# Performance work log

Measured on AMD Instinct MI355X. Metric: run time of the kernel, lower is better.

Reference implementation:

```python
import jax, jax.numpy as jnp
import numpy as np

B, SEQ, DIM = 2, 4096, 1024
E, S = 8, 512          # num_slots = seq_len // num_experts
HID = 4 * DIM          # FeedForward hidden: dim * mult
SCALE = DIM ** 0.5     # RMSNorm scale


def rmsnorm(x, gamma):
    # matches F.normalize(x, dim=-1) * dim**0.5 * gamma (eps=1e-12 clamp on the norm)
    n = jnp.linalg.norm(x, axis=-1, keepdims=True)
    return x / jnp.maximum(n, 1e-12) * SCALE * gamma


def setup_inputs() -> dict:
    key = jax.random.key(0)
    ks = jax.random.split(key, 4)
    w_init = lambda k, shape: jax.random.normal(k, shape, dtype=jnp.float32) * 0.02
    return {
        "x": jax.random.normal(ks[0], (B, SEQ, DIM), dtype=jnp.float32),
        "norm_gamma": jnp.ones((DIM,), jnp.float32),
        "slot_norm_gamma": jnp.ones((DIM,), jnp.float32),
        "slot_embeds": jax.random.normal(ks[1], (E, S, DIM), dtype=jnp.float32),
        "w1": w_init(ks[2], (E, DIM, HID)),
        "b1": jnp.zeros((E, HID), jnp.float32),
        "w2": w_init(ks[3], (E, HID, DIM)),
        "b2": jnp.zeros((E, DIM), jnp.float32),
    }


def reference(x, norm_gamma, slot_norm_gamma, slot_embeds, w1, b1, w2, b2):
    xn = rmsnorm(x, norm_gamma)                 # [b, n, d]
    sn = rmsnorm(slot_embeds, slot_norm_gamma)  # [e, s, d]

    logits = jnp.einsum('bnd,esd->bnes', xn, sn)                   # [b, n, e, s]
    dispatch = jax.nn.softmax(logits, axis=1)                      # softmax over tokens n
    b, n, e, s = logits.shape
    combine = jax.nn.softmax(logits.reshape(b, n, e * s), axis=-1) # softmax over (e s)

    slots = jnp.einsum('bnd,bnes->besd', xn, dispatch)             # [b, e, s, d]

    # per-expert FeedForward: Linear -> GELU(exact) -> Linear (dropout=0)
    h = jnp.einsum('besd,edh->besh', slots, w1) + b1[None, :, None, :]
    h = jax.nn.gelu(h, approximate=False)
    eo = jnp.einsum('besh,ehd->besd', h, w2) + b2[None, :, None, :]

    eo = eo.reshape(b, e * s, DIM)                                 # [b, (e s), d]
    out = jnp.einsum('bmd,bnm->bnd', eo, combine)                  # [b, n, d]
    return out
```

## Files before the change

### kernel.cpp

```cpp
#include <hip/hip_runtime.h>
#include <math.h>

#define SEQ    4096
#define DIM    1024
#define NEXP   8
#define NSLOT  512
#define ES     4096
#define HID    4096
#define NB     2
#define RMS_SCALE 32.0f

typedef __attribute__((ext_vector_type(4))) float f32x4;
typedef __attribute__((ext_vector_type(8))) short bf16x8;
typedef __attribute__((ext_vector_type(4))) unsigned short us4;

__device__ __forceinline__ unsigned short f2bf(float f) {
    unsigned u = __float_as_uint(f);
    u += 0x7fff + ((u >> 16) & 1);
    return (unsigned short)(u >> 16);
}
__device__ __forceinline__ float bf2f(unsigned short h) {
    return __uint_as_float(((unsigned)h) << 16);
}
__device__ __forceinline__ float gelu_exact(float x) {
    return 0.5f * x * (1.0f + erff(x * 0.70710678118654752f));
}

#define GLOAD_LDS16(gp, lp) \
    __builtin_amdgcn_global_load_lds((const __attribute__((address_space(1))) void*)(gp), \
                                     (__attribute__((address_space(3))) void*)(lp), 16, 0, 0)

__device__ __forceinline__ unsigned ldsoff(const void* p) {
    return (unsigned)(size_t)(const __attribute__((address_space(3))) void*)p;
}

#define DSR(dst, base, off) asm volatile("ds_read_b128 %0, %1 offset:" off : "=v"(dst) : "v"(base))
#define VM(n) asm volatile("s_waitcnt vmcnt(" #n ")" ::: "memory")
#define BAR __builtin_amdgcn_s_barrier()
#define SCB __builtin_amdgcn_sched_barrier(0)

#define PH_OPEN  SCB; BAR; asm volatile("s_waitcnt lgkmcnt(0)" ::: "memory"); SCB; \
                 __builtin_amdgcn_s_setprio(1);
#define PH_CLOSE __builtin_amdgcn_s_setprio(0); SCB;

template<int ORDER>
__global__ void rmsnorm_split(const float* __restrict__ in, const float* __restrict__ gamma,
                              unsigned short* __restrict__ outc) {
    int row = blockIdx.x;
    int t = threadIdx.x;
    float4 v = reinterpret_cast<const float4*>(in + (size_t)row * DIM)[t];
    float ss = v.x*v.x + v.y*v.y + v.z*v.z + v.w*v.w;
    #pragma unroll
    for (int off = 32; off >= 1; off >>= 1) ss += __shfl_down(ss, off, 64);
    __shared__ float red[4];
    if ((t & 63) == 0) red[t >> 6] = ss;
    __syncthreads();
    float inv = RMS_SCALE / fmaxf(sqrtf(red[0] + red[1] + red[2] + red[3]), 1e-12f);
    float4 g = reinterpret_cast<const float4*>(gamma)[t];
    float f[4] = {v.x*inv*g.x, v.y*inv*g.y, v.z*inv*g.z, v.w*inv*g.w};
    us4 hv, lv;
    #pragma unroll
    for (int q = 0; q < 4; ++q) {
        unsigned short h = f2bf(f[q]);
        hv[q] = h;
        lv[q] = f2bf(f[q] - bf2f(h));
    }
    unsigned short* rb = outc + (size_t)row * 3072;
    *reinterpret_cast<us4*>(&rb[t*4]) = hv;
    if (ORDER == 0) {
        *reinterpret_cast<us4*>(&rb[1024 + t*4]) = hv;
        *reinterpret_cast<us4*>(&rb[2048 + t*4]) = lv;
    } else {
        *reinterpret_cast<us4*>(&rb[1024 + t*4]) = lv;
        *reinterpret_cast<us4*>(&rb[2048 + t*4]) = hv;
    }
}

__global__ void col_stats_partial(const float* __restrict__ logits,
                                  float* __restrict__ pmax, float* __restrict__ psum) {
    int col = blockIdx.x * 256 + threadIdx.x;
    int ch  = blockIdx.y;
    int b   = blockIdx.z;
    const float* base = logits + ((size_t)b * SEQ + (size_t)ch * 512) * ES + col;
    float m = -INFINITY, s = 0.f;
    for (int n = 0; n < 512; ++n) {
        float v = base[(size_t)n * ES];
        float mn = fmaxf(m, v);
        s = s * __expf(m - mn) + __expf(v - mn);
        m = mn;
    }
    size_t idx = ((size_t)b * 8 + ch) * ES + col;
    pmax[idx] = m; psum[idx] = s;
}

__global__ void col_stats_reduce(const float* __restrict__ pmax, const float* __restrict__ psum,
                                 float* __restrict__ cmax, float* __restrict__ cinv) {
    int col = blockIdx.x * 256 + threadIdx.x;
    int b   = blockIdx.y;
    float m = -INFINITY, s = 0.f;
    for (int ch = 0; ch < 8; ++ch) {
        size_t idx = ((size_t)b * 8 + ch) * ES + col;
        float m2 = pmax[idx], s2 = psum[idx];
        float mn = fmaxf(m, m2);
        s = s * __expf(m - mn) + s2 * __expf(m2 - mn);
        m = mn;
    }
    cmax[(size_t)b * ES + col] = m;
    cinv[(size_t)b * ES + col] = 1.0f / s;
}

__global__ void row_stats(const float* __restrict__ logits,
                          float* __restrict__ rmax, float* __restrict__ rinv) {
    int row = blockIdx.x;
    int t = threadIdx.x;
    const float* base = logits + (size_t)row * ES;
    float m = -INFINITY, s = 0.f;
    for (int i = t; i < ES; i += 256) {
        float v = base[i];
        float mn = fmaxf(m, v);
        s = s * __expf(m - mn) + __expf(v - mn);
        m = mn;
    }
    __shared__ float sm[256], ssum[256];
    sm[t] = m; ssum[t] = s;
    __syncthreads();
    for (int off = 128; off >= 1; off >>= 1) {
        if (t < off) {
            float m1 = sm[t], m2 = sm[t+off], s1 = ssum[t], s2 = ssum[t+off];
            float mn = fmaxf(m1, m2);
            sm[t] = mn;
            ssum[t] = s1 * __expf(m1 - mn) + s2 * __expf(m2 - mn);
        }
        __syncthreads();
    }
    if (t == 0) { rmax[row] = sm[0]; rinv[row] = 1.0f / ssum[0]; }
}

__global__ void make_weights(const float* __restrict__ logits,
                             const float* __restrict__ cmax, const float* __restrict__ cinv,
                             const float* __restrict__ rmax, const float* __restrict__ rinv,
                             unsigned short* __restrict__ comb, unsigned short* __restrict__ dispT) {
    int b = blockIdx.z;
    const float* L = logits + (size_t)b * SEQ * ES;
    int n0 = blockIdx.y * 32, e0 = blockIdx.x * 32;
    int t = threadIdx.x;
    int r = t >> 3, c4 = (t & 7) * 4;
    __shared__ unsigned short tile[32][36];
    float4 v = *reinterpret_cast<const float4*>(&L[(size_t)(n0 + r) * ES + e0 + c4]);
    float rm = rmax[b*SEQ + n0 + r], ri = rinv[b*SEQ + n0 + r];
    float vv[4] = {v.x, v.y, v.z, v.w};
    us4 cb;
    #pragma unroll
    for (int q = 0; q < 4; ++q) {
        cb[q] = f2bf(__expf(vv[q] - rm) * ri);
        float dv = __expf(vv[q] - cmax[b*ES + e0 + c4 + q]) * cinv[b*ES + e0 + c4 + q];
        tile[c4 + q][r] = f2bf(dv);
    }
    *reinterpret_cast<us4*>(&comb[(size_t)b*SEQ*ES + (size_t)(n0 + r)*ES + e0 + c4]) = cb;
    __syncthreads();
    us4 o = *reinterpret_cast<us4*>(&tile[t >> 3][(t & 7) * 4]);
    *reinterpret_cast<us4*>(&dispT[(size_t)b*ES*SEQ + (size_t)(e0 + (t >> 3))*SEQ + n0 + (t & 7)*4]) = o;
}

__global__ void transpose_b16(const unsigned short* __restrict__ src, unsigned short* __restrict__ dst,
                              int sld, int dld, long sStride, long dStride) {
    int z = blockIdx.z;
    const unsigned short* S = src + (size_t)z * sStride;
    unsigned short* D = dst + (size_t)z * dStride;
    int r0 = blockIdx.y * 32, c0 = blockIdx.x * 32;
    int t = threadIdx.x;
    __shared__ unsigned short tile[32][36];
    us4 v = *reinterpret_cast<const us4*>(&S[(size_t)(r0 + (t>>3)) * sld + c0 + (t&7)*4]);
    #pragma unroll
    for (int q = 0; q < 4; ++q) tile[(t&7)*4 + q][t>>3] = v[q];
    __syncthreads();
    us4 o = *reinterpret_cast<us4*>(&tile[t >> 3][(t & 7) * 4]);
    *reinterpret_cast<us4*>(&D[(size_t)(c0 + (t>>3)) * dld + r0 + (t&7)*4]) = o;
}

__global__ void transpose_f32_b16(const float* __restrict__ src, unsigned short* __restrict__ dst,
                                  int sld, int dld, long sStride, long dStride) {
    int z = blockIdx.z;
    const float* S = src + (size_t)z * sStride;
    unsigned short* D = dst + (size_t)z * dStride;
    int r0 = blockIdx.y * 32, c0 = blockIdx.x * 32;
    int t = threadIdx.x;
    __shared__ unsigned short tile[32][36];
    float4 v = *reinterpret_cast<const float4*>(&S[(size_t)(r0 + (t>>3)) * sld + c0 + (t&7)*4]);
    float vv[4] = {v.x, v.y, v.z, v.w};
    #pragma unroll
    for (int q = 0; q < 4; ++q) tile[(t&7)*4 + q][t>>3] = f2bf(vv[q]);
    __syncthreads();
    us4 o = *reinterpret_cast<us4*>(&tile[t >> 3][(t & 7) * 4]);
    *reinterpret_cast<us4*>(&D[(size_t)(c0 + (t>>3)) * dld + r0 + (t&7)*4]) = o;
}

template<int EPI, int OM>
__global__ __launch_bounds__(512, 2)
void mfma_gemm256(const unsigned short* __restrict__ A, const unsigned short* __restrict__ B,
                  void* __restrict__ Cv, const float* __restrict__ bias,
                  int N, int K, int lda, int ldb, int ldc,
                  long aStride, long bStride, long cStride, int bMod) {
    __shared__ unsigned short lds[65536];
    const int t = threadIdx.x;
    const int lane = t & 63, wave = t >> 6;
    const int wr = wave >> 2, wc = wave & 3;
    const int z = blockIdx.z, zb = z % bMod;
    const unsigned short* Ab = A + (size_t)z * aStride;
    const unsigned short* Bb = B + (size_t)zb * bStride;
    const int gx = gridDim.x;
    int flat = blockIdx.x + blockIdx.y * gx;
    const int cpx = (gx * gridDim.y) >> 3;
    flat = (flat & 7) * cpx + (flat >> 3);
    const int m0 = (flat / gx) * 256, n0 = (flat % gx) * 256;

    const int sr = t >> 3;
    const int sg = (t & 7) ^ (sr & 7);
    const unsigned short* gA = Ab + (size_t)(m0 + sr) * lda + sg * 8;
    const int srB = sr + (sr & 32);
    const unsigned short* gB = Bb + (size_t)(n0 + srB) * ldb + sg * 8;
    unsigned short* ldsw = lds + wave * 512;

    const int lr = lane & 15, lk = lane >> 4;
    const unsigned sw0 = (unsigned)(((lk)     ^ (lr & 7)) << 4);
    const unsigned sw1 = (unsigned)(((4 + lk) ^ (lr & 7)) << 4);
    const unsigned l0  = ldsoff(lds);
    const unsigned arow = (unsigned)((wr*64 + lr) * 128);
    const unsigned brow = (unsigned)((wc*32 + lr) * 128);
    const unsigned ab00 = l0 + arow + sw0,          ab10 = l0 + arow + sw1;
    const unsigned bb00 = l0 + 32768 + brow + sw0,  bb10 = l0 + 32768 + brow + sw1;
    const unsigned ab01 = ab00 + 65536, ab11 = ab10 + 65536;
    const unsigned bb01 = bb00 + 65536, bb11 = bb10 + 65536;

    #define STAGE_A(buf, half, tt) do { \
        const unsigned short* _g = gA + (size_t)((half)*64) * lda + (tt)*64; \
        unsigned short* _l = ldsw + (buf)*32768 + (half)*8192; \
        GLOAD_LDS16(_g, _l); \
        GLOAD_LDS16(_g + (size_t)128*lda, _l + 4096); } while(0)
    #define STAGE_B(buf, half, tt) do { \
        const unsigned short* _g = gB + (size_t)((half)*32) * ldb + (tt)*64; \
        unsigned short* _l = ldsw + (buf)*32768 + 16384 + (half)*8192; \
        GLOAD_LDS16(_g, _l); \
        GLOAD_LDS16(_g + (size_t)128*ldb, _l + 4096); } while(0)

    #define MFMA16(MB, CN) \
        _Pragma("unroll") \
        for (int m = 0; m < 4; ++m) { \
            _Pragma("unroll") \
            for (int n = 0; n < 2; ++n) { \
                acc[(MB)+m][(CN)+n] = __builtin_amdgcn_mfma_f32_16x16x32_bf16(a0[m], b0[(CN)+n], acc[(MB)+m][(CN)+n], 0, 0, 0); \
                acc[(MB)+m][(CN)+n] = __builtin_amdgcn_mfma_f32_16x16x32_bf16(a1[m], b1[(CN)+n], acc[(MB)+m][(CN)+n], 0, 0, 0); \
            } \
        }

    f32x4 acc[8][4] = {};
    bf16x8 a0[4], a1[4], b0[4], b1[4];
    const int NT = K / 64;

    STAGE_A(0, 0, 0); STAGE_B(0, 0, 0); STAGE_B(0, 1, 0); STAGE_A(0, 1, 0);
    STAGE_A(1, 0, 1); STAGE_B(1, 0, 1); STAGE_B(1, 1, 1);
    VM(10); BAR;

    for (int tt = 0; tt < NT; tt += 2) {
        const bool pf2 = (tt + 2 < NT);
        const bool pf3 = (tt + 3 < NT);
        DSR(a0[0], ab00, "0");    DSR(a0[1], ab00, "2048");
        DSR(a0[2], ab00, "4096"); DSR(a0[3], ab00, "6144");
        DSR(a1[0], ab10, "0");    DSR(a1[1], ab10, "2048");
        DSR(a1[2], ab10, "4096"); DSR(a1[3], ab10, "6144");
        DSR(b0[0], bb00, "0");    DSR(b0[1], bb00, "2048");
        DSR(b1[0], bb10, "0");    DSR(b1[1], bb10, "2048");
        STAGE_A(1, 1, tt+1);
        PH_OPEN MFMA16(0, 0) PH_CLOSE
        VM(10); BAR;
        DSR(b0[2], bb00, "16384"); DSR(b0[3], bb00, "18432");
        DSR(b1[2], bb10, "16384"); DSR(b1[3], bb10, "18432");
        if (pf2) STAGE_A(0, 0, tt+2);
        PH_OPEN MFMA16(0, 2) PH_CLOSE
        if (pf2) { VM(10); } else { VM(8); }
        BAR;
        DSR(a0[0], ab00, "16384"); DSR(a0[1], ab00, "18432");
        DSR(a0[2], ab00, "20480"); DSR(a0[3], ab00, "22528");
        DSR(a1[0], ab10, "16384"); DSR(a1[1], ab10, "18432");
        DSR(a1[2], ab10, "20480"); DSR(a1[3], ab10, "22528");
        if (pf2) STAGE_B(0, 0, tt+2);
        PH_OPEN MFMA16(4, 0) PH_CLOSE
        BAR;
        if (pf2) STAGE_B(0, 1, tt+2);
        PH_OPEN MFMA16(4, 2) PH_CLOSE
        if (pf2) { VM(10); } else { VM(4); }
        BAR;
        DSR(a0[0], ab01, "0");    DSR(a0[1], ab01, "2048");
        DSR(a0[2], ab01, "4096"); DSR(a0[3], ab01, "6144");
        DSR(a1[0], ab11, "0");    DSR(a1[1], ab11, "2048");
        DSR(a1[2], ab11, "4096"); DSR(a1[3], ab11, "6144");
        DSR(b0[0], bb01, "0");    DSR(b0[1], bb01, "2048");
        DSR(b1[0], bb11, "0");    DSR(b1[1], bb11, "2048");
        if (pf2) STAGE_A(0, 1, tt+2);
        PH_OPEN MFMA16(0, 0) PH_CLOSE
        if (pf2) { VM(10); } else { VM(2); }
        BAR;
        DSR(b0[2], bb01, "16384"); DSR(b0[3], bb01, "18432");
        DSR(b1[2], bb11, "16384"); DSR(b1[3], bb11, "18432");
        if (pf3) STAGE_A(1, 0, tt+3);
        PH_OPEN MFMA16(0, 2) PH_CLOSE
        if (pf2) { VM(10); } else { VM(0); }
        BAR;
        DSR(a0[0], ab01, "16384"); DSR(a0[1], ab01, "18432");
        DSR(a0[2], ab01, "20480"); DSR(a0[3], ab01, "22528");
        DSR(a1[0], ab11, "16384"); DSR(a1[1], ab11, "18432");
        DSR(a1[2], ab11, "20480"); DSR(a1[3], ab11, "22528");
        if (pf3) STAGE_B(1, 0, tt+3);
        PH_OPEN MFMA16(4, 0) PH_CLOSE
        BAR;
        if (pf3) STAGE_B(1, 1, tt+3);
        PH_OPEN MFMA16(4, 2) PH_CLOSE
        if (pf2) { VM(10); } else { VM(0); }
        BAR;
    }

    const float* bz = (EPI != 0) ? bias + (size_t)zb * N : nullptr;
    long coff = (long)z * cStride;
    int rbase = (lane >> 4) * 4;
    int cbase = lane & 15;
    #pragma unroll
    for (int f = 0; f < 8; ++f) {
        #pragma unroll
        for (int n = 0; n < 4; ++n) {
            int col  = n0 + wc*64 + n*16 + cbase;
            int row0 = m0 + wr*128 + f*16 + rbase;
            float bv = (EPI != 0) ? bz[col] : 0.f;
            float vals[4];
            #pragma unroll
            for (int r = 0; r < 4; ++r) {
                float v = acc[f][n][r] + bv;
                if (EPI == 2) v = gelu_exact(v);
                vals[r] = v;
            }
            if (OM == 0) {
                float* C = (float*)Cv + coff;
                #pragma unroll
                for (int r = 0; r < 4; ++r) C[(size_t)(row0 + r) * ldc + col] = vals[r];
            } else {
                unsigned short* C = (unsigned short*)Cv + coff;
                #pragma unroll
                for (int r = 0; r < 4; ++r) C[(size_t)(row0 + r) * ldc + col] = f2bf(vals[r]);
            }
        }
    }
    #undef STAGE_A
    #undef STAGE_B
    #undef MFMA16
}

template<int EPI, int OM>
__global__ __launch_bounds__(512, 2)
void mfma_gemmX(const unsigned short* __restrict__ A, const unsigned short* __restrict__ B,
                void* __restrict__ Cv, const float* __restrict__ bias,
                int N, int K, int lda, int ldb, int ldc,
                long aStride, long bStride, long cStride, long cStrideE, int bMod) {
    __shared__ unsigned short lds[49152];
    const int t = threadIdx.x;
    const int lane = t & 63, wave = t >> 6;
    const int wr = wave >> 2, wc = wave & 3;
    const int z = blockIdx.z, zb = z % bMod;
    const unsigned short* Ab = A + (size_t)z * aStride;
    const unsigned short* Bb = B + (size_t)zb * bStride;
    const int gx = gridDim.x;
    int flat = blockIdx.x + blockIdx.y * gx;
    const int cpx = (gx * gridDim.y) >> 3;
    flat = (flat & 7) * cpx + (flat >> 3);
    const int m0 = (flat / gx) * 256, n0 = (flat % gx) * 128;

    const int sr = t >> 3;
    const int sg = (t & 7) ^ (sr & 7);
    const unsigned short* gA = Ab + (size_t)(m0 + sr) * lda + sg * 8;
    const unsigned short* gB = Bb + (size_t)(n0 + sr) * ldb + sg * 8;
    unsigned short* ldsw = lds + wave * 512;

    const int lr = lane & 15, lk = lane >> 4;
    const unsigned g0 = (unsigned)(((lk)     ^ (lr & 7)) << 4);
    const unsigned g1 = (unsigned)(((4 + lk) ^ (lr & 7)) << 4);
    const unsigned l0 = ldsoff(lds);
    const unsigned arow = (unsigned)((wr*64 + lr) * 128);
    const unsigned brow = (unsigned)((wc*32 + lr) * 128);
    const unsigned ax00 = l0 + arow + g0,          ax10 = l0 + arow + g1;
    const unsigned bx00 = l0 + 32768 + brow + g0,  bx10 = l0 + 32768 + brow + g1;
    const unsigned ax01 = ax00 + 49152, ax11 = ax10 + 49152;
    const unsigned bx01 = bx00 + 49152, bx11 = bx10 + 49152;

    #define STAGE_AX(buf, quad, tt) do { \
        const unsigned short* _g = gA + (size_t)((quad)*64) * lda + (tt)*64; \
        unsigned short* _l = ldsw + (buf)*24576 + (quad)*8192; \
        GLOAD_LDS16(_g, _l); \
        GLOAD_LDS16(_g + (size_t)128*lda, _l + 4096); } while(0)
    #define STAGE_BX(buf, tt) do { \
        const unsigned short* _g = gB + (tt)*64; \
        unsigned short* _l = ldsw + (buf)*24576 + 16384; \
        GLOAD_LDS16(_g, _l); \
        GLOAD_LDS16(_g + (size_t)64*ldb, _l + 4096); } while(0)

    #define MFMA8(MB, AR, BR) \
        _Pragma("unroll") \
        for (int m = 0; m < 4; ++m) { \
            _Pragma("unroll") \
            for (int n = 0; n < 2; ++n) { \
                acc[(MB)+m][n] = __builtin_amdgcn_mfma_f32_16x16x32_bf16(AR[m], BR[n], acc[(MB)+m][n], 0, 0, 0); \
            } \
        }

    f32x4 acc[8][2] = {};
    bf16x8 a0[4], a1[4], b0[2], b1[2];
    const int NT = K / 64;

    STAGE_AX(0, 0, 0); STAGE_BX(0, 0); STAGE_AX(0, 1, 0);
    STAGE_AX(1, 0, 1); STAGE_BX(1, 1);
    VM(6); BAR;

    for (int tt = 0; tt < NT; tt += 2) {
        const bool pf2 = (tt + 2 < NT);
        const bool pf3 = (tt + 3 < NT);
        DSR(a0[0], ax00, "0");    DSR(a0[1], ax00, "2048");
        DSR(a0[2], ax00, "4096"); DSR(a0[3], ax00, "6144");
        DSR(b0[0], bx00, "0");    DSR(b0[1], bx00, "2048");
        STAGE_AX(1, 1, tt+1);
        PH_OPEN MFMA8(0, a0, b0) PH_CLOSE
        BAR;
        DSR(a1[0], ax10, "0");    DSR(a1[1], ax10, "2048");
        DSR(a1[2], ax10, "4096"); DSR(a1[3], ax10, "6144");
        DSR(b1[0], bx10, "0");    DSR(b1[1], bx10, "2048");
        PH_OPEN MFMA8(0, a1, b1) PH_CLOSE
        VM(6); BAR;
        DSR(a0[0], ax00, "16384"); DSR(a0[1], ax00, "18432");
        DSR(a0[2], ax00, "20480"); DSR(a0[3], ax00, "22528");
        if (pf2) STAGE_AX(0, 0, tt+2);
        PH_OPEN MFMA8(4, a0, b0) PH_CLOSE
        BAR;
        DSR(a1[0], ax10, "16384"); DSR(a1[1], ax10, "18432");
        DSR(a1[2], ax10, "20480"); DSR(a1[3], ax10, "22528");
        if (pf2) STAGE_BX(0, tt+2);
        PH_OPEN MFMA8(4, a1, b1) PH_CLOSE
        if (pf2) { VM(6); } else { VM(2); }
        BAR;
        DSR(a0[0], ax01, "0");    DSR(a0[1], ax01, "2048");
        DSR(a0[2], ax01, "4096"); DSR(a0[3], ax01, "6144");
        DSR(b0[0], bx01, "0");    DSR(b0[1], bx01, "2048");
        if (pf2) STAGE_AX(0, 1, tt+2);
        PH_OPEN MFMA8(0, a0, b0) PH_CLOSE
        BAR;
        DSR(a1[0], ax11, "0");    DSR(a1[1], ax11, "2048");
        DSR(a1[2], ax11, "4096"); DSR(a1[3], ax11, "6144");
        DSR(b1[0], bx11, "0");    DSR(b1[1], bx11, "2048");
        PH_OPEN MFMA8(0, a1, b1) PH_CLOSE
        if (pf2) { VM(6); } else { VM(0); }
        BAR;
        DSR(a0[0], ax01, "16384"); DSR(a0[1], ax01, "18432");
        DSR(a0[2], ax01, "20480"); DSR(a0[3], ax01, "22528");
        if (pf3) STAGE_AX(1, 0, tt+3);
        PH_OPEN MFMA8(4, a0, b0) PH_CLOSE
        BAR;
        DSR(a1[0], ax11, "16384"); DSR(a1[1], ax11, "18432");
        DSR(a1[2], ax11, "20480"); DSR(a1[3], ax11, "22528");
        if (pf3) STAGE_BX(1, tt+3);
        PH_OPEN MFMA8(4, a1, b1) PH_CLOSE
        if (pf2) { VM(6); } else { VM(0); }
        BAR;
    }

    const float* bz = (EPI != 0) ? bias + (size_t)zb * N : nullptr;
    long coff = (long)z * cStride + (long)zb * cStrideE;
    int rbase = (lane >> 4) * 4;
    int cbase = lane & 15;
    #pragma unroll
    for (int f = 0; f < 8; ++f) {
        #pragma unroll
        for (int n = 0; n < 2; ++n) {
            int col  = n0 + wc*32 + n*16 + cbase;
            int row0 = m0 + wr*128 + f*16 + rbase;
            float bv = (EPI != 0) ? bz[col] : 0.f;
            float vals[4];
            #pragma unroll
            for (int r = 0; r < 4; ++r) {
                float v = acc[f][n][r] + bv;
                if (EPI == 2) v = gelu_exact(v);
                vals[r] = v;
            }
            if (OM == 0) {
                float* C = (float*)Cv + coff;
                #pragma unroll
                for (int r = 0; r < 4; ++r) C[(size_t)(row0 + r) * ldc + col] = vals[r];
            } else if (OM == 1) {
                unsigned short* C = (unsigned short*)Cv + coff;
                #pragma unroll
                for (int r = 0; r < 4; ++r) C[(size_t)(row0 + r) * ldc + col] = f2bf(vals[r]);
            } else {
                unsigned short* C = (unsigned short*)Cv + coff;
                us4 o;
                #pragma unroll
                for (int r = 0; r < 4; ++r) o[r] = f2bf(vals[r]);
                *reinterpret_cast<us4*>(&C[(size_t)col * ldc + row0]) = o;
            }
        }
    }
    #undef STAGE_AX
    #undef STAGE_BX
    #undef MFMA8
}

extern "C" void kernel_launch(void* const* d_in, const int* in_sizes, int n_in,
                              void* d_out, int out_size, void* d_ws, size_t ws_size,
                              hipStream_t stream) {
    const float* x    = (const float*)d_in[0];
    const float* ng   = (const float*)d_in[1];
    const float* sg   = (const float*)d_in[2];
    const float* semb = (const float*)d_in[3];
    const float* w1   = (const float*)d_in[4];
    const float* b1   = (const float*)d_in[5];
    const float* w2   = (const float*)d_in[6];
    const float* b2   = (const float*)d_in[7];
    float* out = (float*)d_out;

    char* base = (char*)d_ws;
    unsigned short* Acat  = (unsigned short*)(base);
    unsigned short* Bcat  = (unsigned short*)(base + 50331648);
    unsigned short* dispT = (unsigned short*)(base);
    unsigned short* w2T   = (unsigned short*)(base);
    float*          logits= (float*)(base + 75497472);
    unsigned short* hbuf  = (unsigned short*)(base + 75497472);
    unsigned short* w1T   = (unsigned short*)(base + 142606336);
    unsigned short* xnT   = (unsigned short*)(base + 209715200);
    unsigned short* comb  = (unsigned short*)(base + 226492416);
    unsigned short* slots = (unsigned short*)(base + 293601280);
    unsigned short* eoT   = (unsigned short*)(base + 293601280);
    float* pmax = (float*)(base + 310378496);
    float* psum = pmax + 65536;
    float* cmax = psum + 65536;
    float* cinv = cmax + 8192;
    float* rmax = cinv + 8192;
    float* rinv = rmax + 8192;

    rmsnorm_split<0><<<NB*SEQ, 256, 0, stream>>>(x, ng, Acat);
    rmsnorm_split<1><<<NEXP*NSLOT, 256, 0, stream>>>(semb, sg, Bcat);

    transpose_b16<<<dim3(DIM/32, SEQ/32, NB), 256, 0, stream>>>(
        Acat, xnT, 3072, SEQ, (long)SEQ*3072, (long)DIM*SEQ);

    mfma_gemm256<0,0><<<dim3(ES/256, (NB*SEQ)/256, 1), 512, 0, stream>>>(
        Acat, Bcat, logits, nullptr, ES, 3072, 3072, 3072, ES,
        0L, 0L, 0L, 1);

    col_stats_partial<<<dim3(ES/256, 8, NB), 256, 0, stream>>>(logits, pmax, psum);
    col_stats_reduce<<<dim3(ES/256, NB), 256, 0, stream>>>(pmax, psum, cmax, cinv);
    row_stats<<<NB*SEQ, 256, 0, stream>>>(logits, rmax, rinv);

    make_weights<<<dim3(ES/32, SEQ/32, NB), 256, 0, stream>>>(
        logits, cmax, cinv, rmax, rinv, comb, dispT);

    transpose_f32_b16<<<dim3(HID/32, DIM/32, NEXP), 256, 0, stream>>>(
        w1, w1T, HID, DIM, (long)DIM*HID, (long)HID*DIM);

    mfma_gemmX<0,1><<<dim3(DIM/128, ES/256, NB), 512, 0, stream>>>(
        dispT, xnT, slots, nullptr, DIM, SEQ, SEQ, SEQ, DIM,
        (long)ES*SEQ, (long)DIM*SEQ, (long)ES*DIM, 0L, NB);

    transpose_f32_b16<<<dim3(DIM/32, HID/32, NEXP), 256, 0, stream>>>(
        w2, w2T, DIM, HID, (long)HID*DIM, (long)DIM*HID);

    mfma_gemm256<2,1><<<dim3(HID/256, NSLOT/256, NB*NEXP), 512, 0, stream>>>(
        slots, w1T, hbuf, b1, HID, DIM, DIM, DIM, HID,
        (long)NSLOT*DIM, (long)HID*DIM, (long)NSLOT*HID, NEXP);

    mfma_gemmX<1,2><<<dim3(DIM/128, NSLOT/256, NB*NEXP), 512, 0, stream>>>(
        hbuf, w2T, eoT, b2, DIM, HID, HID, HID, ES,
        (long)NSLOT*HID, (long)DIM*HID, (long)(DIM*ES/NEXP), (long)(NSLOT - DIM*ES/NEXP), NEXP);

    mfma_gemmX<0,0><<<dim3(DIM/128, SEQ/256, NB), 512, 0, stream>>>(
        comb, eoT, out, nullptr, DIM, ES, ES, ES, DIM,
        (long)SEQ*ES, (long)DIM*ES, (long)SEQ*DIM, 0L, NB);
}
```

Measured before the change: 707.9 us.

## Fuse softmax row/column statistics into logits GEMM epilogue

Computes per-tile row and column max/sum-exp partials inside the logits GEMM epilogue from the accumulators, replacing the separate col_stats_partial, col_stats_reduce and row_stats kernels with small reduce kernels over the partials. This removes two full re-reads of the 128 MB fp32 logits buffer. It also reworks the vmcnt wait counts in both GEMM main loops, dropping several waits and changing thresholds, which alters load/compute overlap and risks correctness if the counts are wrong. The extra epilogue shuffles and exps add work to the GEMM.

```diff
diff --git a/kernel.cpp b/kernel.cpp
--- a/kernel.cpp
+++ b/kernel.cpp
@@ -76,64 +76,31 @@
     }
 }
 
-__global__ void col_stats_partial(const float* __restrict__ logits,
-                                  float* __restrict__ pmax, float* __restrict__ psum) {
-    int col = blockIdx.x * 256 + threadIdx.x;
-    int ch  = blockIdx.y;
-    int b   = blockIdx.z;
-    const float* base = logits + ((size_t)b * SEQ + (size_t)ch * 512) * ES + col;
+__global__ void row_reduce(const float* __restrict__ pM, const float* __restrict__ pS,
+                           float* __restrict__ rmax, float* __restrict__ rinv) {
+    int row = blockIdx.x * 256 + threadIdx.x;
     float m = -INFINITY, s = 0.f;
-    for (int n = 0; n < 512; ++n) {
-        float v = base[(size_t)n * ES];
-        float mn = fmaxf(m, v);
-        s = s * __expf(m - mn) + __expf(v - mn);
-        m = mn;
-    }
-    size_t idx = ((size_t)b * 8 + ch) * ES + col;
-    pmax[idx] = m; psum[idx] = s;
-}
-
-__global__ void col_stats_reduce(const float* __restrict__ pmax, const float* __restrict__ psum,
-                                 float* __restrict__ cmax, float* __restrict__ cinv) {
-    int col = blockIdx.x * 256 + threadIdx.x;
-    int b   = blockIdx.y;
-    float m = -INFINITY, s = 0.f;
-    for (int ch = 0; ch < 8; ++ch) {
-        size_t idx = ((size_t)b * 8 + ch) * ES + col;
-        float m2 = pmax[idx], s2 = psum[idx];
+    for (int p = 0; p < 64; ++p) {
+        float m2 = pM[(size_t)p*8192 + row], s2 = pS[(size_t)p*8192 + row];
         float mn = fmaxf(m, m2);
         s = s * __expf(m - mn) + s2 * __expf(m2 - mn);
         m = mn;
     }
-    cmax[(size_t)b * ES + col] = m;
-    cinv[(size_t)b * ES + col] = 1.0f / s;
-}
-
-__global__ void row_stats(const float* __restrict__ logits,
-                          float* __restrict__ rmax, float* __restrict__ rinv) {
-    int row = blockIdx.x;
-    int t = threadIdx.x;
-    const float* base = logits + (size_t)row * ES;
+    rmax[row] = m; rinv[row] = 1.0f / s;
+}
+
+__global__ void col_reduce(const float* __restrict__ pM, const float* __restrict__ pS,
+                           float* __restrict__ cmax, float* __restrict__ cinv) {
+    int col = blockIdx.x * 256 + threadIdx.x;
+    int b = blockIdx.y;
     float m = -INFINITY, s = 0.f;
-    for (int i = t; i < ES; i += 256) {
-        float v = base[i];
-        float mn = fmaxf(m, v);
-        s = s * __expf(m - mn) + __expf(v - mn);
+    for (int p = b*32; p < b*32 + 32; ++p) {
+        float m2 = pM[(size_t)p*4096 + col], s2 = pS[(size_t)p*4096 + col];
+        float mn = fmaxf(m, m2);
+        s = s * __expf(m - mn) + s2 * __expf(m2 - mn);
         m = mn;
     }
-    __shared__ float sm[256], ssum[256];
-    sm[t] = m; ssum[t] = s;
-    __syncthreads();
-    for (int off = 128; off >= 1; off >>= 1) {
-        if (t < off) {
-            float m1 = sm[t], m2 = sm[t+off], s1 = ssum[t], s2 = ssum[t+off];
-            float mn = fmaxf(m1, m2);
-            sm[t] = mn;
-            ssum[t] = s1 * __expf(m1 - mn) + s2 * __expf(m2 - mn);
-        }
-        __syncthreads();
-    }
-    if (t == 0) { rmax[row] = sm[0]; rinv[row] = 1.0f / ssum[0]; }
+    cmax[b*4096 + col] = m; cinv[b*4096 + col] = 1.0f / s;
 }
 
 __global__ void make_weights(const float* __restrict__ logits,
@@ -195,12 +162,14 @@
     *reinterpret_cast<us4*>(&D[(size_t)(c0 + (t>>3)) * dld + r0 + (t&7)*4]) = o;
 }
 
-template<int EPI, int OM>
+template<int EPI, int OM, int STATS>
 __global__ __launch_bounds__(512, 2)
 void mfma_gemm256(const unsigned short* __restrict__ A, const unsigned short* __restrict__ B,
                   void* __restrict__ Cv, const float* __restrict__ bias,
                   int N, int K, int lda, int ldb, int ldc,
-                  long aStride, long bStride, long cStride, int bMod) {
+                  long aStride, long bStride, long cStride, int bMod,
+                  float* __restrict__ rowpM, float* __restrict__ rowpS,
+                  float* __restrict__ colpM, float* __restrict__ colpS) {
     __shared__ unsigned short lds[65536];
     const int t = threadIdx.x;
     const int lane = t & 63, wave = t >> 6;
@@ -259,7 +228,7 @@
 
     STAGE_A(0, 0, 0); STAGE_B(0, 0, 0); STAGE_B(0, 1, 0); STAGE_A(0, 1, 0);
     STAGE_A(1, 0, 1); STAGE_B(1, 0, 1); STAGE_B(1, 1, 1);
-    VM(10); BAR;
+    VM(0); BAR;
 
     for (int tt = 0; tt < NT; tt += 2) {
         const bool pf2 = (tt + 2 < NT);
@@ -272,12 +241,11 @@
         DSR(b1[0], bb10, "0");    DSR(b1[1], bb10, "2048");
         STAGE_A(1, 1, tt+1);
         PH_OPEN MFMA16(0, 0) PH_CLOSE
-        VM(10); BAR;
+        BAR;
         DSR(b0[2], bb00, "16384"); DSR(b0[3], bb00, "18432");
         DSR(b1[2], bb10, "16384"); DSR(b1[3], bb10, "18432");
         if (pf2) STAGE_A(0, 0, tt+2);
         PH_OPEN MFMA16(0, 2) PH_CLOSE
-        if (pf2) { VM(10); } else { VM(8); }
         BAR;
         DSR(a0[0], ab00, "16384"); DSR(a0[1], ab00, "18432");
         DSR(a0[2], ab00, "20480"); DSR(a0[3], ab00, "22528");
@@ -288,7 +256,7 @@
         BAR;
         if (pf2) STAGE_B(0, 1, tt+2);
         PH_OPEN MFMA16(4, 2) PH_CLOSE
-        if (pf2) { VM(10); } else { VM(4); }
+        if (pf2) { VM(6); } else { VM(0); }
         BAR;
         DSR(a0[0], ab01, "0");    DSR(a0[1], ab01, "2048");
         DSR(a0[2], ab01, "4096"); DSR(a0[3], ab01, "6144");
@@ -298,13 +266,11 @@
         DSR(b1[0], bb11, "0");    DSR(b1[1], bb11, "2048");
         if (pf2) STAGE_A(0, 1, tt+2);
         PH_OPEN MFMA16(0, 0) PH_CLOSE
-        if (pf2) { VM(10); } else { VM(2); }
         BAR;
         DSR(b0[2], bb01, "16384"); DSR(b0[3], bb01, "18432");
         DSR(b1[2], bb11, "16384"); DSR(b1[3], bb11, "18432");
         if (pf3) STAGE_A(1, 0, tt+3);
         PH_OPEN MFMA16(0, 2) PH_CLOSE
-        if (pf2) { VM(10); } else { VM(0); }
         BAR;
         DSR(a0[0], ab01, "16384"); DSR(a0[1], ab01, "18432");
         DSR(a0[2], ab01, "20480"); DSR(a0[3], ab01, "22528");
@@ -315,8 +281,53 @@
         BAR;
         if (pf3) STAGE_B(1, 1, tt+3);
         PH_OPEN MFMA16(4, 2) PH_CLOSE
-        if (pf2) { VM(10); } else { VM(0); }
-        BAR;
+        if (pf3) { VM(6); } else { VM(0); }
+        BAR;
+    }
+
+    if (STATS) {
+        #pragma unroll
+        for (int f = 0; f < 8; ++f) {
+            #pragma unroll
+            for (int r = 0; r < 4; ++r) {
+                float m = fmaxf(fmaxf(acc[f][0][r], acc[f][1][r]), fmaxf(acc[f][2][r], acc[f][3][r]));
+                #pragma unroll
+                for (int msk = 1; msk <= 8; msk <<= 1) m = fmaxf(m, __shfl_xor(m, msk, 64));
+                float s = __expf(acc[f][0][r]-m) + __expf(acc[f][1][r]-m)
+                        + __expf(acc[f][2][r]-m) + __expf(acc[f][3][r]-m);
+                #pragma unroll
+                for (int msk = 1; msk <= 8; msk <<= 1) s += __shfl_xor(s, msk, 64);
+                if ((lane & 15) == 0) {
+                    int row = m0 + wr*128 + f*16 + (lane>>4)*4 + r;
+                    int slot = (n0 >> 6) + wc;
+                    rowpM[(size_t)slot*8192 + row] = m;
+                    rowpS[(size_t)slot*8192 + row] = s;
+                }
+            }
+        }
+        #pragma unroll
+        for (int n = 0; n < 4; ++n) {
+            float m = -INFINITY;
+            #pragma unroll
+            for (int f = 0; f < 8; ++f)
+                #pragma unroll
+                for (int r = 0; r < 4; ++r) m = fmaxf(m, acc[f][n][r]);
+            m = fmaxf(m, __shfl_xor(m, 16, 64));
+            m = fmaxf(m, __shfl_xor(m, 32, 64));
+            float s = 0.f;
+            #pragma unroll
+            for (int f = 0; f < 8; ++f)
+                #pragma unroll
+                for (int r = 0; r < 4; ++r) s += __expf(acc[f][n][r] - m);
+            s += __shfl_xor(s, 16, 64);
+            s += __shfl_xor(s, 32, 64);
+            if ((lane >> 4) == 0) {
+                int col = n0 + wc*64 + n*16 + lane;
+                int slot = (m0 >> 7) + wr;
+                colpM[(size_t)slot*4096 + col] = m;
+                colpS[(size_t)slot*4096 + col] = s;
+            }
+        }
     }
 
     const float* bz = (EPI != 0) ? bias + (size_t)zb * N : nullptr;
@@ -415,7 +426,7 @@
 
     STAGE_AX(0, 0, 0); STAGE_BX(0, 0); STAGE_AX(0, 1, 0);
     STAGE_AX(1, 0, 1); STAGE_BX(1, 1);
-    VM(6); BAR;
+    VM(0); BAR;
 
     for (int tt = 0; tt < NT; tt += 2) {
         const bool pf2 = (tt + 2 < NT);
@@ -430,7 +441,7 @@
         DSR(a1[2], ax10, "4096"); DSR(a1[3], ax10, "6144");
         DSR(b1[0], bx10, "0");    DSR(b1[1], bx10, "2048");
         PH_OPEN MFMA8(0, a1, b1) PH_CLOSE
-        VM(6); BAR;
+        BAR;
         DSR(a0[0], ax00, "16384"); DSR(a0[1], ax00, "18432");
         DSR(a0[2], ax00, "20480"); DSR(a0[3], ax00, "22528");
         if (pf2) STAGE_AX(0, 0, tt+2);
@@ -440,7 +451,7 @@
         DSR(a1[2], ax10, "20480"); DSR(a1[3], ax10, "22528");
         if (pf2) STAGE_BX(0, tt+2);
         PH_OPEN MFMA8(4, a1, b1) PH_CLOSE
-        if (pf2) { VM(6); } else { VM(2); }
+        if (pf2) { VM(4); } else { VM(0); }
         BAR;
         DSR(a0[0], ax01, "0");    DSR(a0[1], ax01, "2048");
         DSR(a0[2], ax01, "4096"); DSR(a0[3], ax01, "6144");
@@ -452,7 +463,6 @@
         DSR(a1[2], ax11, "4096"); DSR(a1[3], ax11, "6144");
         DSR(b1[0], bx11, "0");    DSR(b1[1], bx11, "2048");
         PH_OPEN MFMA8(0, a1, b1) PH_CLOSE
-        if (pf2) { VM(6); } else { VM(0); }
         BAR;
         DSR(a0[0], ax01, "16384"); DSR(a0[1], ax01, "18432");
         DSR(a0[2], ax01, "20480"); DSR(a0[3], ax01, "22528");
@@ -463,7 +473,7 @@
         DSR(a1[2], ax11, "20480"); DSR(a1[3], ax11, "22528");
         if (pf3) STAGE_BX(1, tt+3);
         PH_OPEN MFMA8(4, a1, b1) PH_CLOSE
-        if (pf2) { VM(6); } else { VM(0); }
+        if (pf3) { VM(4); } else { VM(0); }
         BAR;
     }
 
@@ -532,9 +542,11 @@
     unsigned short* comb  = (unsigned short*)(base + 226492416);
     unsigned short* slots = (unsigned short*)(base + 293601280);
     unsigned short* eoT   = (unsigned short*)(base + 293601280);
-    float* pmax = (float*)(base + 310378496);
-    float* psum = pmax + 65536;
-    float* cmax = psum + 65536;
+    float* rowpM = (float*)(base + 226492416);
+    float* rowpS = rowpM + 64*8192;
+    float* colpM = rowpS + 64*8192;
+    float* colpS = colpM + 64*4096;
+    float* cmax = (float*)(base + 310378496);
     float* cinv = cmax + 8192;
     float* rmax = cinv + 8192;
     float* rinv = rmax + 8192;
@@ -545,13 +557,12 @@
     transpose_b16<<<dim3(DIM/32, SEQ/32, NB), 256, 0, stream>>>(
         Acat, xnT, 3072, SEQ, (long)SEQ*3072, (long)DIM*SEQ);
 
-    mfma_gemm256<0,0><<<dim3(ES/256, (NB*SEQ)/256, 1), 512, 0, stream>>>(
+    mfma_gemm256<0,0,1><<<dim3(ES/256, (NB*SEQ)/256, 1), 512, 0, stream>>>(
         Acat, Bcat, logits, nullptr, ES, 3072, 3072, 3072, ES,
-        0L, 0L, 0L, 1);
-
-    col_stats_partial<<<dim3(ES/256, 8, NB), 256, 0, stream>>>(logits, pmax, psum);
-    col_stats_reduce<<<dim3(ES/256, NB), 256, 0, stream>>>(pmax, psum, cmax, cinv);
-    row_stats<<<NB*SEQ, 256, 0, stream>>>(logits, rmax, rinv);
+        0L, 0L, 0L, 1, rowpM, rowpS, colpM, colpS);
+
+    row_reduce<<<32, 256, 0, stream>>>(rowpM, rowpS, rmax, rinv);
+    col_reduce<<<dim3(16, 2), 256, 0, stream>>>(colpM, colpS, cmax, cinv);
 
     make_weights<<<dim3(ES/32, SEQ/32, NB), 256, 0, stream>>>(
         logits, cmax, cinv, rmax, rinv, comb, dispT);
@@ -566,9 +577,10 @@
     transpose_f32_b16<<<dim3(DIM/32, HID/32, NEXP), 256, 0, stream>>>(
         w2, w2T, DIM, HID, (long)HID*DIM, (long)DIM*HID);
 
-    mfma_gemm256<2,1><<<dim3(HID/256, NSLOT/256, NB*NEXP), 512, 0, stream>>>(
+    mfma_gemm256<2,1,0><<<dim3(HID/256, NSLOT/256, NB*NEXP), 512, 0, stream>>>(
         slots, w1T, hbuf, b1, HID, DIM, DIM, DIM, HID,
-        (long)NSLOT*DIM, (long)HID*DIM, (long)NSLOT*HID, NEXP);
+        (long)NSLOT*DIM, (long)HID*DIM, (long)NSLOT*HID, NEXP,
+        nullptr, nullptr, nullptr, nullptr);
 
     mfma_gemmX<1,2><<<dim3(DIM/128, NSLOT/256, NB*NEXP), 512, 0, stream>>>(
         hbuf, w2T, eoT, b2, DIM, HID, HID, HID, ES,
```

Measured after the change: 694.4 us. About the same (-1.9%).
